# Kernel tuning notes

Hardware: AMD Instinct MI355X
Metric: run time of the kernel (lower is better)

Reference implementation:

```python
import jax, jax.numpy as jnp
import numpy as np

U, I, D = 100000, 50000, 64   # num_users, num_items, embedding_dim
B = 16384                      # batch of (user, item) queries
T = 3000000                    # total implicit interactions (ragged, CSR-style)
GLOBAL_MEAN = 3.5


def setup_inputs() -> dict:
    key = jax.random.key(0)
    ks = jax.random.split(key, 9)
    user_idx = jax.random.randint(ks[0], (B,), 0, U)
    item_idx = jax.random.randint(ks[1], (B,), 0, I)
    flat_items = jax.random.randint(ks[2], (T,), 0, I)
    segment_ids = jnp.sort(jax.random.randint(ks[3], (T,), 0, U))
    user_factors = 0.01 * jax.random.normal(ks[4], (U, D), dtype=jnp.float32)
    item_factors = 0.01 * jax.random.normal(ks[5], (I, D), dtype=jnp.float32)
    item_implicit_factors = 0.01 * jax.random.normal(ks[6], (I, D), dtype=jnp.float32)
    user_bias = jnp.zeros((U,), dtype=jnp.float32)
    item_bias = jnp.zeros((I,), dtype=jnp.float32)
    global_mean = jnp.float32(GLOBAL_MEAN)
    return {
        "user_idx": user_idx, "item_idx": item_idx,
        "flat_items": flat_items, "segment_ids": segment_ids,
        "user_factors": user_factors, "item_factors": item_factors,
        "item_implicit_factors": item_implicit_factors,
        "user_bias": user_bias, "item_bias": item_bias,
        "global_mean": global_mean,
    }


def reference(user_idx, item_idx, flat_items, segment_ids,
              user_factors, item_factors, item_implicit_factors,
              user_bias, item_bias, global_mean):
    num_users = user_factors.shape[0]
    # sum_{j in N(u)} y_j  for all users in one segment reduction  -> [U, D]
    y = item_implicit_factors[flat_items]                      # [T, D] gather
    agg = jax.ops.segment_sum(y, segment_ids, num_segments=num_users)
    counts = jax.ops.segment_sum(jnp.ones_like(segment_ids, dtype=y.dtype),
                                 segment_ids, num_segments=num_users)
    inv_sqrt = jnp.where(counts > 0, jax.lax.rsqrt(jnp.maximum(counts, 1.0)), 0.0)
    agg = agg * inv_sqrt[:, None]                              # |N(u)|^{-1/2} * sum y_j

    p_u = user_factors[user_idx]                               # [B, D]
    q_i = item_factors[item_idx]                               # [B, D]
    implicit_u = agg[user_idx]                                 # [B, D]
    dot = jnp.sum((p_u + implicit_u) * q_i, axis=-1)           # [B]
    return global_mean + user_bias[user_idx] + item_bias[item_idx] + dot
```

## Files before the change

### kernel.cpp

```cpp
#include <hip/hip_runtime.h>
#include <hip/hip_bf16.h>

#define DIM 64

__global__ void svdpp_boundaries(const int* __restrict__ seg_ids,
                                 int* __restrict__ row_start,
                                 int* __restrict__ row_end, int T) {
    long t = (long)(blockIdx.x * blockDim.x + threadIdx.x) * 4;
    if (t >= T) return;
    int lane = threadIdx.x & 63;

    int s0, s1, s2, s3;
    if (t + 3 < T) {
        int4 v = *(const int4*)(seg_ids + t);
        s0 = v.x; s1 = v.y; s2 = v.z; s3 = v.w;
    } else {
        s0 = seg_ids[t];
        s1 = (t + 1 < T) ? seg_ids[t + 1] : s0;
        s2 = (t + 2 < T) ? seg_ids[t + 2] : s1;
        s3 = (t + 3 < T) ? seg_ids[t + 3] : s2;
    }

    int prev = __shfl_up(s3, 1, 64);
    if (lane == 0) prev = (t > 0) ? seg_ids[t - 1] : -1;

    if (t == 0) row_start[s0] = 0;
    else if (s0 != prev) { row_start[s0] = (int)t; row_end[prev] = (int)t; }
    if (t + 1 < T && s1 != s0) { row_start[s1] = (int)t + 1; row_end[s0] = (int)t + 1; }
    if (t + 2 < T && s2 != s1) { row_start[s2] = (int)t + 2; row_end[s1] = (int)t + 2; }
    if (t + 3 < T && s3 != s2) { row_start[s3] = (int)t + 3; row_end[s2] = (int)t + 3; }

    if      (t + 3 == T - 1) row_end[s3] = T;
    else if (t + 2 == T - 1) row_end[s2] = T;
    else if (t + 1 == T - 1) row_end[s1] = T;
    else if (t     == T - 1) row_end[s0] = T;
}

__global__ void svdpp_fused(const int* __restrict__ user_idx,
                            const int* __restrict__ item_idx,
                            const int* __restrict__ flat_items,
                            const float* __restrict__ user_factors,
                            const float* __restrict__ item_factors,
                            const float* __restrict__ imp,
                            const int* __restrict__ row_start,
                            const int* __restrict__ row_end,
                            const float* __restrict__ user_bias,
                            const float* __restrict__ item_bias,
                            const float* __restrict__ gm,
                            float* __restrict__ out, int B) {
    int w = (blockIdx.x * blockDim.x + threadIdx.x) >> 6;
    int lane = threadIdx.x & 63;
    if (w >= B) return;
    int sub = lane & 15;
    int grp = lane >> 4;

    int u = user_idx[w];
    int i = item_idx[w];
    int s0 = row_start[u];
    int s1 = row_end[u];
    if (s0 < 0) { s0 = 0; s1 = 0; }

    float4 p4 = *(const float4*)(user_factors + (long)u * DIM + sub * 4);
    float4 q4 = *(const float4*)(item_factors + (long)i * DIM + sub * 4);

    float4 accA = {0.f, 0.f, 0.f, 0.f};
    float4 accB = {0.f, 0.f, 0.f, 0.f};

    for (long base = s0; base < s1; base += 64) {
        int rem = (int)(s1 - base);
        if (rem > 64) rem = 64;
        int items = (lane < rem) ? flat_items[base + lane] : 0;

        int k = 0;
        for (; k + 8 <= rem; k += 8) {
            int ia = __shfl(items, k + grp, 64);
            int ib = __shfl(items, k + 4 + grp, 64);
            float4 ra = *(const float4*)(imp + (long)ia * DIM + sub * 4);
            float4 rb = *(const float4*)(imp + (long)ib * DIM + sub * 4);
            accA.x += ra.x; accA.y += ra.y; accA.z += ra.z; accA.w += ra.w;
            accB.x += rb.x; accB.y += rb.y; accB.z += rb.z; accB.w += rb.w;
        }
        for (; k < rem; k += 4) {
            int kk = k + grp;
            bool val = kk < rem;
            int ic = __shfl(items, val ? kk : 0, 64);
            float4 rc = *(const float4*)(imp + (long)ic * DIM + sub * 4);
            if (val) {
                accA.x += rc.x; accA.y += rc.y; accA.z += rc.z; accA.w += rc.w;
            }
        }
    }

    int n = s1 - s0;
    float inv = (n > 0) ? rsqrtf((float)n) : 0.f;

    float ax = accA.x + accB.x, ay = accA.y + accB.y;
    float az = accA.z + accB.z, aw = accA.w + accB.w;
    float v = inv * (ax * q4.x + ay * q4.y + az * q4.z + aw * q4.w);
    if (grp == 0)
        v += p4.x * q4.x + p4.y * q4.y + p4.z * q4.z + p4.w * q4.w;

    #pragma unroll
    for (int off = 32; off >= 1; off >>= 1)
        v += __shfl_down(v, off, 64);

    if (lane == 0)
        out[w] = gm[0] + user_bias[u] + item_bias[i] + v;
}

extern "C" void kernel_launch(void* const* d_in, const int* in_sizes, int n_in,
                              void* d_out, int out_size, void* d_ws, size_t ws_size,
                              hipStream_t stream) {
    const int*   user_idx     = (const int*)d_in[0];
    const int*   item_idx     = (const int*)d_in[1];
    const int*   flat_items   = (const int*)d_in[2];
    const int*   seg_ids      = (const int*)d_in[3];
    const float* user_factors = (const float*)d_in[4];
    const float* item_factors = (const float*)d_in[5];
    const float* imp          = (const float*)d_in[6];
    const float* user_bias    = (const float*)d_in[7];
    const float* item_bias    = (const float*)d_in[8];
    const float* gm           = (const float*)d_in[9];
    float* out = (float*)d_out;

    const int B = in_sizes[0];
    const int T = in_sizes[2];
    const int U = in_sizes[7];

    int* row_start = (int*)d_ws;
    int* row_end   = row_start + U;

    const int n4 = (T + 3) / 4;
    svdpp_boundaries<<<(n4 + 255) / 256, 256, 0, stream>>>(seg_ids, row_start,
                                                           row_end, T);

    svdpp_fused<<<(B + 3) / 4, 256, 0, stream>>>(user_idx, item_idx,
                                                 flat_items, user_factors,
                                                 item_factors, imp,
                                                 row_start, row_end,
                                                 user_bias, item_bias,
                                                 gm, out, B);
}
```

Before: 130.1 us.

## Replace boundary-scan kernel with per-query binary search over sorted segment ids

Removes the separate kernel that scanned all 3M segment ids to build row_start/row_end tables. Each query wavefront instead binary-searches the sorted seg_ids for the lower bounds of u and u+1, using about 22 dependent loads per query instead of a full pass over T. The gather loop is also unrolled to 16 rows per step with four accumulators to keep more loads in flight. The trade-off is serial latency on dependent global loads inside the main kernel, in exchange for dropping a bandwidth-bound pre-pass and a kernel launch. It also removes the bug where stale workspace values were read for users with no interactions.

```diff
diff --git a/kernel.cpp b/kernel.cpp
--- a/kernel.cpp
+++ b/kernel.cpp
@@ -3,51 +3,17 @@
 
 #define DIM 64
 
-__global__ void svdpp_boundaries(const int* __restrict__ seg_ids,
-                                 int* __restrict__ row_start,
-                                 int* __restrict__ row_end, int T) {
-    long t = (long)(blockIdx.x * blockDim.x + threadIdx.x) * 4;
-    if (t >= T) return;
-    int lane = threadIdx.x & 63;
-
-    int s0, s1, s2, s3;
-    if (t + 3 < T) {
-        int4 v = *(const int4*)(seg_ids + t);
-        s0 = v.x; s1 = v.y; s2 = v.z; s3 = v.w;
-    } else {
-        s0 = seg_ids[t];
-        s1 = (t + 1 < T) ? seg_ids[t + 1] : s0;
-        s2 = (t + 2 < T) ? seg_ids[t + 2] : s1;
-        s3 = (t + 3 < T) ? seg_ids[t + 3] : s2;
-    }
-
-    int prev = __shfl_up(s3, 1, 64);
-    if (lane == 0) prev = (t > 0) ? seg_ids[t - 1] : -1;
-
-    if (t == 0) row_start[s0] = 0;
-    else if (s0 != prev) { row_start[s0] = (int)t; row_end[prev] = (int)t; }
-    if (t + 1 < T && s1 != s0) { row_start[s1] = (int)t + 1; row_end[s0] = (int)t + 1; }
-    if (t + 2 < T && s2 != s1) { row_start[s2] = (int)t + 2; row_end[s1] = (int)t + 2; }
-    if (t + 3 < T && s3 != s2) { row_start[s3] = (int)t + 3; row_end[s2] = (int)t + 3; }
-
-    if      (t + 3 == T - 1) row_end[s3] = T;
-    else if (t + 2 == T - 1) row_end[s2] = T;
-    else if (t + 1 == T - 1) row_end[s1] = T;
-    else if (t     == T - 1) row_end[s0] = T;
-}
-
 __global__ void svdpp_fused(const int* __restrict__ user_idx,
                             const int* __restrict__ item_idx,
                             const int* __restrict__ flat_items,
+                            const int* __restrict__ seg_ids,
                             const float* __restrict__ user_factors,
                             const float* __restrict__ item_factors,
                             const float* __restrict__ imp,
-                            const int* __restrict__ row_start,
-                            const int* __restrict__ row_end,
                             const float* __restrict__ user_bias,
                             const float* __restrict__ item_bias,
                             const float* __restrict__ gm,
-                            float* __restrict__ out, int B) {
+                            float* __restrict__ out, int B, int T) {
     int w = (blockIdx.x * blockDim.x + threadIdx.x) >> 6;
     int lane = threadIdx.x & 63;
     if (w >= B) return;
@@ -56,15 +22,26 @@
 
     int u = user_idx[w];
     int i = item_idx[w];
-    int s0 = row_start[u];
-    int s1 = row_end[u];
-    if (s0 < 0) { s0 = 0; s1 = 0; }
+
+    int lo0 = 0, hi0 = T;
+    int lo1 = 0, hi1 = T;
+    while ((lo0 < hi0) | (lo1 < hi1)) {
+        int m0 = (lo0 + hi0) >> 1;
+        int m1 = (lo1 + hi1) >> 1;
+        int v0 = (lo0 < hi0) ? seg_ids[m0] : 0;
+        int v1 = (lo1 < hi1) ? seg_ids[m1] : 0;
+        if (lo0 < hi0) { if (v0 < u)     lo0 = m0 + 1; else hi0 = m0; }
+        if (lo1 < hi1) { if (v1 < u + 1) lo1 = m1 + 1; else hi1 = m1; }
+    }
+    int s0 = lo0, s1 = lo1;
 
     float4 p4 = *(const float4*)(user_factors + (long)u * DIM + sub * 4);
     float4 q4 = *(const float4*)(item_factors + (long)i * DIM + sub * 4);
 
     float4 accA = {0.f, 0.f, 0.f, 0.f};
     float4 accB = {0.f, 0.f, 0.f, 0.f};
+    float4 accC = {0.f, 0.f, 0.f, 0.f};
+    float4 accD = {0.f, 0.f, 0.f, 0.f};
 
     for (long base = s0; base < s1; base += 64) {
         int rem = (int)(s1 - base);
@@ -72,6 +49,20 @@
         int items = (lane < rem) ? flat_items[base + lane] : 0;
 
         int k = 0;
+        for (; k + 16 <= rem; k += 16) {
+            int ia = __shfl(items, k + grp, 64);
+            int ib = __shfl(items, k + 4 + grp, 64);
+            int ic = __shfl(items, k + 8 + grp, 64);
+            int id = __shfl(items, k + 12 + grp, 64);
+            float4 ra = *(const float4*)(imp + (long)ia * DIM + sub * 4);
+            float4 rb = *(const float4*)(imp + (long)ib * DIM + sub * 4);
+            float4 rc = *(const float4*)(imp + (long)ic * DIM + sub * 4);
+            float4 rd = *(const float4*)(imp + (long)id * DIM + sub * 4);
+            accA.x += ra.x; accA.y += ra.y; accA.z += ra.z; accA.w += ra.w;
+            accB.x += rb.x; accB.y += rb.y; accB.z += rb.z; accB.w += rb.w;
+            accC.x += rc.x; accC.y += rc.y; accC.z += rc.z; accC.w += rc.w;
+            accD.x += rd.x; accD.y += rd.y; accD.z += rd.z; accD.w += rd.w;
+        }
         for (; k + 8 <= rem; k += 8) {
             int ia = __shfl(items, k + grp, 64);
             int ib = __shfl(items, k + 4 + grp, 64);
@@ -94,8 +85,10 @@
     int n = s1 - s0;
     float inv = (n > 0) ? rsqrtf((float)n) : 0.f;
 
-    float ax = accA.x + accB.x, ay = accA.y + accB.y;
-    float az = accA.z + accB.z, aw = accA.w + accB.w;
+    float ax = accA.x + accB.x + accC.x + accD.x;
+    float ay = accA.y + accB.y + accC.y + accD.y;
+    float az = accA.z + accB.z + accC.z + accD.z;
+    float aw = accA.w + accB.w + accC.w + accD.w;
     float v = inv * (ax * q4.x + ay * q4.y + az * q4.z + aw * q4.w);
     if (grp == 0)
         v += p4.x * q4.x + p4.y * q4.y + p4.z * q4.z + p4.w * q4.w;
@@ -125,19 +118,10 @@
 
     const int B = in_sizes[0];
     const int T = in_sizes[2];
-    const int U = in_sizes[7];
-
-    int* row_start = (int*)d_ws;
-    int* row_end   = row_start + U;
-
-    const int n4 = (T + 3) / 4;
-    svdpp_boundaries<<<(n4 + 255) / 256, 256, 0, stream>>>(seg_ids, row_start,
-                                                           row_end, T);
 
     svdpp_fused<<<(B + 3) / 4, 256, 0, stream>>>(user_idx, item_idx,
-                                                 flat_items, user_factors,
-                                                 item_factors, imp,
-                                                 row_start, row_end,
-                                                 user_bias, item_bias,
-                                                 gm, out, B);
+                                                 flat_items, seg_ids,
+                                                 user_factors, item_factors,
+                                                 imp, user_bias, item_bias,
+                                                 gm, out, B, T);
 }
```

Result: slower. 141.1 us (+8.5%).
